# Kernel optimization log

Measured on AMD Instinct MI355X. Metric: run time of the kernel, lower is better.

Reference implementation:

```python
import jax, jax.numpy as jnp
import numpy as np

N_EXPERTS = 8
D_HEAD = 64  # scaling dim (per-expert sub-dim)


def setup_inputs() -> dict:
    key = jax.random.key(0)
    k1, k2, k3, k4, k5, k6 = jax.random.split(key, 6)
    B, H, T, D = 2, 8, 2048, 512
    Q = jax.random.normal(k1, (B, H, T, D), dtype=jnp.float32)
    K = jax.random.normal(k2, (B, H, T, D), dtype=jnp.float32)
    V = jax.random.normal(k3, (B, H, T, D), dtype=jnp.float32)
    route_mat = jax.random.uniform(k4, (B, N_EXPERTS), dtype=jnp.float32)
    ids = jax.random.randint(k5, (B, N_EXPERTS), 0, 8, dtype=jnp.int32)
    mask = jax.random.randint(k6, (T, T), 0, 2, dtype=jnp.int32)
    return {"Q": Q, "K": K, "V": V, "route_mat": route_mat, "ids": ids, "mask": mask}


def reference(Q, K, V, route_mat, ids, mask):
    B, H, T, D = Q.shape
    E = N_EXPERTS
    ds = D // E
    # split feature dim into expert sub-slices: [B,H,T,E,ds]
    Qe = Q.reshape(B, H, T, E, ds)
    Ke = K.reshape(B, H, T, E, ds)
    Ve = V.reshape(B, H, T, E, ds)
    gate = route_mat[:, None, None, :, None]  # [B,1,1,E,1]
    # Row-parallel routed QK^T: sum over experts of gated partial products.
    dot = jnp.einsum('bhqed,bhked->bhqk', Qe * gate, Ke) / np.sqrt(D_HEAD).astype(np.float32)
    dot = jnp.where(mask[None, None, :, :].astype(bool), -jnp.inf, dot)
    attn = jax.nn.softmax(dot, axis=-1)  # dropout p=0.0 (eval)
    # Column-parallel routed score@V: per-expert output gated, concatenated along feature dim.
    Xe = jnp.einsum('bhqk,bhked->bhqed', attn, Ve) * gate
    return Xe.reshape(B, H, T, D)
```

## Files before the change

kernel.cpp:

```cpp
#include <hip/hip_runtime.h>
#include <stdint.h>

#define T_SEQ 2048
#define D_DIM 512
#define NEXP 8

typedef short bf16x8 __attribute__((ext_vector_type(8)));
typedef float floatx4 __attribute__((ext_vector_type(4)));

__device__ __forceinline__ unsigned short f2bf(float f) {
  union { float f; unsigned u; } v; v.f = f;
  return (unsigned short)((v.u + 0x7fffu + ((v.u >> 16) & 1u)) >> 16);
}

__device__ __forceinline__ void gll16(const void* gsrc, void* ldst) {
  __builtin_amdgcn_global_load_lds(
      (const __attribute__((address_space(1))) unsigned int*)gsrc,
      (__attribute__((address_space(3))) unsigned int*)ldst, 16, 0, 0);
}

__global__ __launch_bounds__(256) void prep_k(const float* __restrict__ K,
                                              unsigned short* __restrict__ kws) {
  int idx = blockIdx.x * 256 + threadIdx.x;
  int r = idx >> 6;
  int c = idx & 63;
  const float4* src = (const float4*)(K + ((long)r << 9) + (c << 3));
  float4 a = src[0], b = src[1];
  bf16x8 v;
  v[0]=f2bf(a.x); v[1]=f2bf(a.y); v[2]=f2bf(a.z); v[3]=f2bf(a.w);
  v[4]=f2bf(b.x); v[5]=f2bf(b.y); v[6]=f2bf(b.z); v[7]=f2bf(b.w);
  int pos = (c ^ (r & 7)) << 4;
  *(bf16x8*)((char*)kws + ((long)r << 10) + pos) = v;
}

__global__ __launch_bounds__(256) void prep_vt(const float* __restrict__ V,
                                               unsigned short* __restrict__ vt) {
  __shared__ unsigned short tile[64][72];
  int bid = blockIdx.x;
  int bh = bid >> 8;
  int kt = (bid >> 3) & 31;
  int dt = bid & 7;
  int k0 = kt << 6, d0 = dt << 6;
  int tid = threadIdx.x;
  {
    int kl = tid >> 2, dc = (tid & 3) << 4;
    const float4* src = (const float4*)(V + ((long)(bh * T_SEQ + k0 + kl) << 9) + d0 + dc);
#pragma unroll
    for (int i = 0; i < 4; ++i) {
      float4 a = src[i];
      tile[kl][dc + 4*i + 0] = f2bf(a.x);
      tile[kl][dc + 4*i + 1] = f2bf(a.y);
      tile[kl][dc + 4*i + 2] = f2bf(a.z);
      tile[kl][dc + 4*i + 3] = f2bf(a.w);
    }
  }
  __syncthreads();
  {
    int dl = tid >> 2, kc = (tid & 3) << 4;
    int d = d0 + dl;
    int swz = ((d ^ (d >> 2)) & 3) << 4;
    long rowbase = (long)(bh * 512 + d) << 12;
#pragma unroll
    for (int m = 0; m < 2; ++m) {
      bf16x8 v;
#pragma unroll
      for (int j = 0; j < 8; ++j) v[j] = tile[kc + 8*m + j][dl];
      int ks = k0 + kc + 8*m;
      int pos = ((ks >> 5) << 6) + ((((ks & 31) << 1)) ^ swz);
      *(bf16x8*)((char*)vt + rowbase + pos) = v;
    }
  }
}

__global__ __launch_bounds__(512, 2) void attn_main(
    const float* __restrict__ Q, const float* __restrict__ route,
    const int* __restrict__ mask, const unsigned short* __restrict__ kws,
    const unsigned short* __restrict__ vtw, float* __restrict__ out) {
  __shared__ __align__(16) char lds[141312];
  const int tid = threadIdx.x;
  const int wq = tid >> 6;
  const int lane = tid & 63;
  const int lq = lane & 15;
  const int g = lane >> 4;
  const int bh = blockIdx.x & 15;
  const int qb = blockIdx.x >> 4;
  const int qw = qb * 128 + wq * 16;
  const int b = bh >> 3;

  float g8[NEXP];
#pragma unroll
  for (int e = 0; e < NEXP; ++e) g8[e] = route[b * NEXP + e];

  bf16x8 qa[16];
  {
    const float* qrow = Q + ((long)(bh * T_SEQ + qw + lq) << 9) + g * 8;
#pragma unroll
    for (int t = 0; t < 16; ++t) {
      const float4* p = (const float4*)(qrow + t * 32);
      float4 a = p[0], c = p[1];
      float sc = g8[t >> 1] * 0.125f;
      qa[t][0]=f2bf(a.x*sc); qa[t][1]=f2bf(a.y*sc); qa[t][2]=f2bf(a.z*sc); qa[t][3]=f2bf(a.w*sc);
      qa[t][4]=f2bf(c.x*sc); qa[t][5]=f2bf(c.y*sc); qa[t][6]=f2bf(c.z*sc); qa[t][7]=f2bf(c.w*sc);
    }
  }

  floatx4 acc[32];
#pragma unroll
  for (int n = 0; n < 32; ++n) acc[n] = 0.f;
  float mrun[4] = {-3e38f, -3e38f, -3e38f, -3e38f};
  float lrun[4] = {0.f, 0.f, 0.f, 0.f};

  const char* kbase = (const char*)kws + ((long)bh << 21);
  const char* vbase = (const char*)vtw + ((long)bh << 21);
  const int swzK = (lq & 7) << 4;
  const int swzA = ((lq ^ (lq >> 2)) & 3) << 4;
  char* pbase = lds + 131072 + wq * 1280;

#define STAGE(buf, K0)                                                          \
  {                                                                             \
    char* kb_ = lds + (buf) * 65536;                                            \
    char* vb_ = kb_ + 32768;                                                    \
    _Pragma("unroll")                                                           \
    for (int r = 0; r < 4; ++r) {                                               \
      int row = 4 * wq + r;                                                     \
      gll16(kbase + ((long)((K0) + row) << 10) + lane * 16, kb_ + row * 1024);  \
    }                                                                           \
    _Pragma("unroll")                                                           \
    for (int r = 0; r < 4; ++r) {                                               \
      int dr0 = 64 * wq + 16 * r;                                               \
      gll16(vbase + ((long)(dr0 + (lane >> 2)) << 12) + (K0) * 2 + (lane & 3) * 16, \
            vb_ + dr0 * 64);                                                    \
    }                                                                           \
  }

  STAGE(0, 0)
  asm volatile("s_waitcnt vmcnt(0)" ::: "memory");
  __syncthreads();

  for (int kt = 0; kt < T_SEQ / 32; ++kt) {
    const int cur = kt & 1;
    const int k0 = kt * 32;
    char* kb = lds + cur * 65536;
    char* vb = kb + 32768;

    if (kt + 1 < T_SEQ / 32) {
      STAGE(cur ^ 1, k0 + 32)
    }

    int mv0[4], mv1[4];
#pragma unroll
    for (int j = 0; j < 4; ++j) {
      long mr = (long)(qw + 4 * g + j) * T_SEQ + k0;
      mv0[j] = mask[mr + lq];
      mv1[j] = mask[mr + 16 + lq];
    }

    floatx4 s0 = 0.f, s1 = 0.f;
#pragma unroll
    for (int t = 0; t < 16; ++t) {
      int off = (t * 64 + g * 16) ^ swzK;
      bf16x8 kf0 = *(const bf16x8*)(kb + lq * 1024 + off);
      bf16x8 kf1 = *(const bf16x8*)(kb + (16 + lq) * 1024 + off);
      s0 = __builtin_amdgcn_mfma_f32_16x16x32_bf16(qa[t], kf0, s0, 0, 0, 0);
      s1 = __builtin_amdgcn_mfma_f32_16x16x32_bf16(qa[t], kf1, s1, 0, 0, 0);
    }

    float tmv[4];
    int grow = 0;
#pragma unroll
    for (int j = 0; j < 4; ++j) {
      if (mv0[j]) s0[j] = -3e38f;
      if (mv1[j]) s1[j] = -3e38f;
      float tm = fmaxf(s0[j], s1[j]);
      tm = fmaxf(tm, __shfl_xor(tm, 1));
      tm = fmaxf(tm, __shfl_xor(tm, 2));
      tm = fmaxf(tm, __shfl_xor(tm, 4));
      tm = fmaxf(tm, __shfl_xor(tm, 8));
      tmv[j] = tm;
      grow |= (tm > mrun[j] + 8.0f) ? 1 : 0;
    }
    if (__any(grow)) {
      float al[4];
#pragma unroll
      for (int j = 0; j < 4; ++j) {
        float mn = fmaxf(mrun[j], tmv[j]);
        al[j] = __expf(mrun[j] - mn);
        mrun[j] = mn;
        lrun[j] *= al[j];
      }
#pragma unroll
      for (int n = 0; n < 32; ++n) {
#pragma unroll
        for (int j = 0; j < 4; ++j) acc[n][j] *= al[j];
      }
    }
#pragma unroll
    for (int j = 0; j < 4; ++j) {
      float p0 = __expf(s0[j] - mrun[j]);
      float p1 = __expf(s1[j] - mrun[j]);
      s0[j] = p0; s1[j] = p1;
      float rs = p0 + p1;
      rs += __shfl_xor(rs, 1);
      rs += __shfl_xor(rs, 2);
      rs += __shfl_xor(rs, 4);
      rs += __shfl_xor(rs, 8);
      lrun[j] += rs;
    }

#pragma unroll
    for (int j = 0; j < 4; ++j) {
      int q = 4 * g + j;
      int swzP = ((q ^ (q >> 2)) & 3) << 4;
      *(unsigned short*)(pbase + q * 80 + ((2 * lq) ^ swzP))      = f2bf(s0[j]);
      *(unsigned short*)(pbase + q * 80 + ((32 + 2 * lq) ^ swzP)) = f2bf(s1[j]);
    }
    bf16x8 pa = *(const bf16x8*)(pbase + lq * 80 + ((16 * g) ^ swzA));
#pragma unroll
    for (int n = 0; n < 32; ++n) {
      int d = 16 * n + lq;
      int swzV = ((d ^ (d >> 2)) & 3) << 4;
      bf16x8 vb8 = *(const bf16x8*)(vb + d * 64 + ((16 * g) ^ swzV));
      acc[n] = __builtin_amdgcn_mfma_f32_16x16x32_bf16(pa, vb8, acc[n], 0, 0, 0);
    }

    asm volatile("s_waitcnt vmcnt(0)" ::: "memory");
    __syncthreads();
  }

  float rl[4];
#pragma unroll
  for (int j = 0; j < 4; ++j) rl[j] = 1.0f / lrun[j];
#pragma unroll
  for (int n = 0; n < 32; ++n) {
    int d = 16 * n + lq;
    float gg = g8[n >> 2];
    float* op = out + ((long)(bh * T_SEQ + qw + 4 * g) << 9) + d;
#pragma unroll
    for (int j = 0; j < 4; ++j) op[(long)j << 9] = acc[n][j] * rl[j] * gg;
  }
}

extern "C" void kernel_launch(void* const* d_in, const int* in_sizes, int n_in,
                              void* d_out, int out_size, void* d_ws, size_t ws_size,
                              hipStream_t stream) {
  (void)in_sizes; (void)n_in; (void)out_size; (void)ws_size;
  const float* Q     = (const float*)d_in[0];
  const float* K     = (const float*)d_in[1];
  const float* V     = (const float*)d_in[2];
  const float* route = (const float*)d_in[3];
  const int*   mask  = (const int*)d_in[5];
  float* out = (float*)d_out;
  unsigned short* kws = (unsigned short*)d_ws;
  unsigned short* vtw = (unsigned short*)((char*)d_ws + 33554432);
  prep_k  <<<8192, 256, 0, stream>>>(K, kws);
  prep_vt <<<4096, 256, 0, stream>>>(V, vtw);
  attn_main<<<256, 512, 0, stream>>>(Q, route, mask, kws, vtw, out);
}
```

Baseline: 633.3 us.

## Software-pipeline QK^T of next tile with softmax and PV of current tile

Restructures the flash-attention main loop so the QK^T MFMAs and mask loads for tile kt+1 are issued before the PV MFMAs of tile kt, and the prefetch of tile kt+2 is staged into the buffer just consumed. The goal is to overlap softmax latency and global loads with matrix-core work and to hide more memory latency. In exchange it holds extra score and mask registers live, which raises register pressure, and it changes where barriers sit in the loop.

```diff
diff --git a/kernel.cpp b/kernel.cpp
--- a/kernel.cpp
+++ b/kernel.cpp
@@ -133,45 +133,45 @@
     }                                                                           \
   }
 
+#define QK16(KB, S0, S1)                                                        \
+  _Pragma("unroll")                                                             \
+  for (int t = 0; t < 16; ++t) {                                                \
+    int off = (t * 64 + g * 16) ^ swzK;                                         \
+    bf16x8 kf0 = *(const bf16x8*)((KB) + lq * 1024 + off);                      \
+    bf16x8 kf1 = *(const bf16x8*)((KB) + (16 + lq) * 1024 + off);               \
+    S0 = __builtin_amdgcn_mfma_f32_16x16x32_bf16(qa[t], kf0, S0, 0, 0, 0);      \
+    S1 = __builtin_amdgcn_mfma_f32_16x16x32_bf16(qa[t], kf1, S1, 0, 0, 0);      \
+  }
+
+#define MASKLOAD(K0, M0, M1)                                                    \
+  _Pragma("unroll")                                                             \
+  for (int j = 0; j < 4; ++j) {                                                 \
+    long mr = (long)(qw + 4 * g + j) * T_SEQ + (K0);                            \
+    M0[j] = mask[mr + lq];                                                      \
+    M1[j] = mask[mr + 16 + lq];                                                 \
+  }
+
   STAGE(0, 0)
+  int mvA0[4], mvA1[4], mvB0[4], mvB1[4];
+  MASKLOAD(0, mvA0, mvA1)
   asm volatile("s_waitcnt vmcnt(0)" ::: "memory");
   __syncthreads();
+  floatx4 sA0 = 0.f, sA1 = 0.f;
+  QK16(lds, sA0, sA1)
+  STAGE(1, 32)
 
   for (int kt = 0; kt < T_SEQ / 32; ++kt) {
     const int cur = kt & 1;
-    const int k0 = kt * 32;
-    char* kb = lds + cur * 65536;
-    char* vb = kb + 32768;
-
-    if (kt + 1 < T_SEQ / 32) {
-      STAGE(cur ^ 1, k0 + 32)
-    }
-
-    int mv0[4], mv1[4];
-#pragma unroll
-    for (int j = 0; j < 4; ++j) {
-      long mr = (long)(qw + 4 * g + j) * T_SEQ + k0;
-      mv0[j] = mask[mr + lq];
-      mv1[j] = mask[mr + 16 + lq];
-    }
-
-    floatx4 s0 = 0.f, s1 = 0.f;
-#pragma unroll
-    for (int t = 0; t < 16; ++t) {
-      int off = (t * 64 + g * 16) ^ swzK;
-      bf16x8 kf0 = *(const bf16x8*)(kb + lq * 1024 + off);
-      bf16x8 kf1 = *(const bf16x8*)(kb + (16 + lq) * 1024 + off);
-      s0 = __builtin_amdgcn_mfma_f32_16x16x32_bf16(qa[t], kf0, s0, 0, 0, 0);
-      s1 = __builtin_amdgcn_mfma_f32_16x16x32_bf16(qa[t], kf1, s1, 0, 0, 0);
-    }
+    char* kb_next = lds + (cur ^ 1) * 65536;
+    char* vb_cur  = lds + cur * 65536 + 32768;
 
     float tmv[4];
     int grow = 0;
 #pragma unroll
     for (int j = 0; j < 4; ++j) {
-      if (mv0[j]) s0[j] = -3e38f;
-      if (mv1[j]) s1[j] = -3e38f;
-      float tm = fmaxf(s0[j], s1[j]);
+      if (mvA0[j]) sA0[j] = -3e38f;
+      if (mvA1[j]) sA1[j] = -3e38f;
+      float tm = fmaxf(sA0[j], sA1[j]);
       tm = fmaxf(tm, __shfl_xor(tm, 1));
       tm = fmaxf(tm, __shfl_xor(tm, 2));
       tm = fmaxf(tm, __shfl_xor(tm, 4));
@@ -196,9 +196,9 @@
     }
 #pragma unroll
     for (int j = 0; j < 4; ++j) {
-      float p0 = __expf(s0[j] - mrun[j]);
-      float p1 = __expf(s1[j] - mrun[j]);
-      s0[j] = p0; s1[j] = p1;
+      float p0 = __expf(sA0[j] - mrun[j]);
+      float p1 = __expf(sA1[j] - mrun[j]);
+      sA0[j] = p0; sA1[j] = p1;
       float rs = p0 + p1;
       rs += __shfl_xor(rs, 1);
       rs += __shfl_xor(rs, 2);
@@ -206,25 +206,39 @@
       rs += __shfl_xor(rs, 8);
       lrun[j] += rs;
     }
-
 #pragma unroll
     for (int j = 0; j < 4; ++j) {
       int q = 4 * g + j;
       int swzP = ((q ^ (q >> 2)) & 3) << 4;
-      *(unsigned short*)(pbase + q * 80 + ((2 * lq) ^ swzP))      = f2bf(s0[j]);
-      *(unsigned short*)(pbase + q * 80 + ((32 + 2 * lq) ^ swzP)) = f2bf(s1[j]);
+      *(unsigned short*)(pbase + q * 80 + ((2 * lq) ^ swzP))      = f2bf(sA0[j]);
+      *(unsigned short*)(pbase + q * 80 + ((32 + 2 * lq) ^ swzP)) = f2bf(sA1[j]);
     }
     bf16x8 pa = *(const bf16x8*)(pbase + lq * 80 + ((16 * g) ^ swzA));
+
+    floatx4 sB0 = 0.f, sB1 = 0.f;
+    if (kt < T_SEQ / 32 - 1) {
+      asm volatile("s_waitcnt vmcnt(0)" ::: "memory");
+      __syncthreads();
+      QK16(kb_next, sB0, sB1)
+      MASKLOAD(kt * 32 + 32, mvB0, mvB1)
+    }
+
 #pragma unroll
     for (int n = 0; n < 32; ++n) {
       int d = 16 * n + lq;
       int swzV = ((d ^ (d >> 2)) & 3) << 4;
-      bf16x8 vb8 = *(const bf16x8*)(vb + d * 64 + ((16 * g) ^ swzV));
+      bf16x8 vb8 = *(const bf16x8*)(vb_cur + d * 64 + ((16 * g) ^ swzV));
       acc[n] = __builtin_amdgcn_mfma_f32_16x16x32_bf16(pa, vb8, acc[n], 0, 0, 0);
     }
 
-    asm volatile("s_waitcnt vmcnt(0)" ::: "memory");
-    __syncthreads();
+    if (kt < T_SEQ / 32 - 2) {
+      __syncthreads();
+      STAGE(cur, kt * 32 + 64)
+    }
+
+    sA0 = sB0; sA1 = sB1;
+#pragma unroll
+    for (int j = 0; j < 4; ++j) { mvA0[j] = mvB0[j]; mvA1[j] = mvB1[j]; }
   }
 
   float rl[4];
```

Result: slower. 788.0 us (+24.4%).
